# Kernel optimization log

Measured on AMD Instinct MI355X. Metric: run time of the kernel, lower is better.

The kernel has to match this reference:

```python
import jax, jax.numpy as jnp
import numpy as np

EMBED_DIM = 512
NUM_HEADS = 8
TGT_LEN = 2048
SRC_LEN = 2048
BSZ = 4
W_SCALE = 0.02  # keep pre-softmax logits in a sane range


def setup_inputs() -> dict:
    key = jax.random.key(0)
    ks = jax.random.split(key, 13)
    E = EMBED_DIM
    inp = {
        "query": jax.random.normal(ks[0], (TGT_LEN, BSZ, E), jnp.float32),
        "key": jax.random.normal(ks[1], (SRC_LEN, BSZ, E), jnp.float32),
        "value": jax.random.normal(ks[2], (SRC_LEN, BSZ, E), jnp.float32),
        "attn_mask": jax.random.normal(ks[3], (TGT_LEN, SRC_LEN), jnp.float32),
        # Linear params, torch layout: W is [out, in], y = x @ W.T + b
        "Wq": jax.random.normal(ks[4], (E, E), jnp.float32) * W_SCALE,
        "bq": jax.random.normal(ks[5], (E,), jnp.float32) * W_SCALE,
        "Wk": jax.random.normal(ks[6], (E, E), jnp.float32) * W_SCALE,
        "bk": jax.random.normal(ks[7], (E,), jnp.float32) * W_SCALE,
        "Wv": jax.random.normal(ks[8], (E, E), jnp.float32) * W_SCALE,
        "bv": jax.random.normal(ks[9], (E,), jnp.float32) * W_SCALE,
        "Wo": jax.random.normal(ks[10], (E, E), jnp.float32) * W_SCALE,
        "bo": jax.random.normal(ks[11], (E,), jnp.float32) * W_SCALE,
    }
    return inp


def reference(query, key, value, attn_mask, Wq, bq, Wk, bk, Wv, bv, Wo, bo):
    # QAT quant/dequant stubs are identity in float math; dropout p=0 (eval) is identity.
    T, B, E = query.shape
    S = key.shape[0]
    H = NUM_HEADS
    hd = E // H
    scale = hd ** (-0.5)

    q = query @ Wq.T + bq            # [T, B, E]
    k = key @ Wk.T + bk              # [S, B, E]
    v = value @ Wv.T + bv            # [S, B, E]

    q = q.reshape(T, B, H, hd) * scale
    k = k.reshape(S, B, H, hd)
    v = v.reshape(S, B, H, hd)

    # scores: [B, H, T, S]
    scores = jnp.einsum("tbhd,sbhd->bhts", q, k)
    scores = scores + attn_mask[None, None, :, :]  # mask_add.add (float mask)
    attn = jax.nn.softmax(scores, axis=-1)         # SegmentLUTSoftmax == softmax in float

    out = jnp.einsum("bhts,sbhd->tbhd", attn, v).reshape(T, B, E)
    out = out @ Wo.T + bo                          # out_proj

    # need_weights=True, average_attn_weights=True: mean over heads -> [B, T, S]
    attn_weights = jnp.sum(attn, axis=1) * (1.0 / H)
    return out, attn_weights
```

## Files before the change

kernel.cpp:

```cpp
#include <hip/hip_runtime.h>
#include <hip/hip_bf16.h>

#define T_LEN 2048
#define S_LEN 2048
#define BSZ   4
#define EMB   512
#define NHEAD 8
#define HDIM  64

using bf16x8 = __attribute__((ext_vector_type(8))) short;
using f32x4  = __attribute__((ext_vector_type(4))) float;

static __device__ __forceinline__ unsigned short f2bf(float x) {
    __hip_bfloat16 h = __float2bfloat16(x);
    return *reinterpret_cast<unsigned short*>(&h);
}
static __device__ __forceinline__ float bf2f(unsigned short u) {
    __hip_bfloat16 h;
    *reinterpret_cast<unsigned short*>(&h) = u;
    return __bfloat162float(h);
}
static __device__ __forceinline__ unsigned int pk2(float a, float b) {
    return (unsigned)f2bf(a) | ((unsigned)f2bf(b) << 16);
}

__global__ __launch_bounds__(256) void convert_w4(
    const float* __restrict__ W0, const float* __restrict__ W1,
    const float* __restrict__ W2, const float* __restrict__ W3,
    unsigned short* __restrict__ Hi, unsigned short* __restrict__ Lo, int n4)
{
    const int z = blockIdx.y;
    const float* X = (z == 0) ? W0 : (z == 1) ? W1 : (z == 2) ? W2 : W3;
    unsigned short* H = Hi + (size_t)z * (size_t)EMB * EMB;
    unsigned short* L = Lo + (size_t)z * (size_t)EMB * EMB;
    const int stride = gridDim.x * 256;
    for (int i = blockIdx.x * 256 + threadIdx.x; i < n4; i += stride) {
        float4 v = ((const float4*)X)[i];
        unsigned short h0 = f2bf(v.x), h1 = f2bf(v.y), h2 = f2bf(v.z), h3 = f2bf(v.w);
        uint2 ph, pg;
        ph.x = (unsigned)h0 | ((unsigned)h1 << 16);
        ph.y = (unsigned)h2 | ((unsigned)h3 << 16);
        pg.x = pk2(v.x - bf2f(h0), v.y - bf2f(h1));
        pg.y = pk2(v.z - bf2f(h2), v.w - bf2f(h3));
        ((uint2*)H)[i] = ph;
        ((uint2*)L)[i] = pg;
    }
}

template <int MODE, bool XF32, bool SPLIT>
__global__ __launch_bounds__(256) void proj_mfma(
    const float* __restrict__ Xf,
    const unsigned short* __restrict__ Xhi, const unsigned short* __restrict__ Xlo,
    const unsigned short* __restrict__ Whi, const unsigned short* __restrict__ Wlo,
    const float* __restrict__ bias,
    float* __restrict__ Yf, unsigned short* __restrict__ Yhi, float scale)
{
    const int n0 = blockIdx.x * 64;
    const int m0 = blockIdx.y * 64;

    __shared__ unsigned short whs[64 * 64];
    __shared__ unsigned short wls[SPLIT ? 64 * 64 : 1];
    __shared__ unsigned short xhs[XF32 ? 64 * 64 : 1];
    __shared__ unsigned short xls[(XF32 && SPLIT) ? 64 * 64 : 1];

    const int tid = threadIdx.x;
    const int w   = tid >> 6;
    const int l   = tid & 63;
    const int l4  = l >> 4, l15 = l & 15;
    const int sw  = (l & 7) << 4;
    char* whsb = (char*)whs;
    char* wlsb = (char*)wls;
    char* xhsb = (char*)xhs;
    char* xlsb = (char*)xls;

    const int srow = tid >> 2;
    const int schk = tid & 3;
    const size_t wbase = (size_t)(n0 + srow) * 512 + schk * 16;
    const int stw = (srow * 128 + schk * 32) ^ ((srow & 7) << 4);

    f32x4 acc[4];
    #pragma unroll
    for (int nb = 0; nb < 4; ++nb) { f32x4 z = {0.f, 0.f, 0.f, 0.f}; acc[nb] = z; }

    uint4 wh0 = *(const uint4*)(Whi + wbase);
    uint4 wh1 = *(const uint4*)(Whi + wbase + 8);
    uint4 wl0, wl1;
    if constexpr (SPLIT) {
        wl0 = *(const uint4*)(Wlo + wbase);
        wl1 = *(const uint4*)(Wlo + wbase + 8);
    }

    const size_t xfbase = (size_t)(m0 + srow) * 512 + schk * 16;
    const size_t xbase  = (size_t)(m0 + w * 16 + l15) * 512 + l4 * 8;
    float4 xp0, xp1, xp2, xp3;
    bf16x8 ah0, ah1, al0, al1;
    if constexpr (XF32) {
        xp0 = *(const float4*)(Xf + xfbase);
        xp1 = *(const float4*)(Xf + xfbase + 4);
        xp2 = *(const float4*)(Xf + xfbase + 8);
        xp3 = *(const float4*)(Xf + xfbase + 12);
    } else {
        ah0 = *(const bf16x8*)(Xhi + xbase);
        ah1 = *(const bf16x8*)(Xhi + xbase + 32);
        if constexpr (SPLIT) {
            al0 = *(const bf16x8*)(Xlo + xbase);
            al1 = *(const bf16x8*)(Xlo + xbase + 32);
        }
    }

    for (int c = 0; c < 8; ++c) {
        __syncthreads();
        *(uint4*)(whsb + stw)        = wh0;
        *(uint4*)(whsb + (stw ^ 16)) = wh1;
        if constexpr (SPLIT) {
            *(uint4*)(wlsb + stw)        = wl0;
            *(uint4*)(wlsb + (stw ^ 16)) = wl1;
        }
        if constexpr (XF32) {
            uint4 H0, H1;
            H0.x = pk2(xp0.x, xp0.y); H0.y = pk2(xp0.z, xp0.w);
            H0.z = pk2(xp1.x, xp1.y); H0.w = pk2(xp1.z, xp1.w);
            H1.x = pk2(xp2.x, xp2.y); H1.y = pk2(xp2.z, xp2.w);
            H1.z = pk2(xp3.x, xp3.y); H1.w = pk2(xp3.z, xp3.w);
            *(uint4*)(xhsb + stw)        = H0;
            *(uint4*)(xhsb + (stw ^ 16)) = H1;
            if constexpr (SPLIT) {
                uint4 L0, L1;
                L0.x = pk2(xp0.x - bf2f(f2bf(xp0.x)), xp0.y - bf2f(f2bf(xp0.y)));
                L0.y = pk2(xp0.z - bf2f(f2bf(xp0.z)), xp0.w - bf2f(f2bf(xp0.w)));
                L0.z = pk2(xp1.x - bf2f(f2bf(xp1.x)), xp1.y - bf2f(f2bf(xp1.y)));
                L0.w = pk2(xp1.z - bf2f(f2bf(xp1.z)), xp1.w - bf2f(f2bf(xp1.w)));
                L1.x = pk2(xp2.x - bf2f(f2bf(xp2.x)), xp2.y - bf2f(f2bf(xp2.y)));
                L1.y = pk2(xp2.z - bf2f(f2bf(xp2.z)), xp2.w - bf2f(f2bf(xp2.w)));
                L1.z = pk2(xp3.x - bf2f(f2bf(xp3.x)), xp3.y - bf2f(f2bf(xp3.y)));
                L1.w = pk2(xp3.z - bf2f(f2bf(xp3.z)), xp3.w - bf2f(f2bf(xp3.w)));
                *(uint4*)(xlsb + stw)        = L0;
                *(uint4*)(xlsb + (stw ^ 16)) = L1;
            }
        }
        __syncthreads();

        bf16x8 cah[2], cal[2];
        if constexpr (XF32) {
            #pragma unroll
            for (int kc = 0; kc < 2; ++kc) {
                const int aoff = (((w * 16 + l15) * 128) + kc * 64 + l4 * 16) ^ sw;
                cah[kc] = *(const bf16x8*)(xhsb + aoff);
                if constexpr (SPLIT) cal[kc] = *(const bf16x8*)(xlsb + aoff);
            }
        } else {
            cah[0] = ah0; cah[1] = ah1;
            if constexpr (SPLIT) { cal[0] = al0; cal[1] = al1; }
        }

        if (c < 7) {
            const size_t wb2 = wbase + (size_t)(c + 1) * 64;
            wh0 = *(const uint4*)(Whi + wb2);
            wh1 = *(const uint4*)(Whi + wb2 + 8);
            if constexpr (SPLIT) {
                wl0 = *(const uint4*)(Wlo + wb2);
                wl1 = *(const uint4*)(Wlo + wb2 + 8);
            }
            if constexpr (XF32) {
                const size_t xb2 = xfbase + (size_t)(c + 1) * 64;
                xp0 = *(const float4*)(Xf + xb2);
                xp1 = *(const float4*)(Xf + xb2 + 4);
                xp2 = *(const float4*)(Xf + xb2 + 8);
                xp3 = *(const float4*)(Xf + xb2 + 12);
            } else {
                const size_t xb2 = xbase + (size_t)(c + 1) * 64;
                ah0 = *(const bf16x8*)(Xhi + xb2);
                ah1 = *(const bf16x8*)(Xhi + xb2 + 32);
                if constexpr (SPLIT) {
                    al0 = *(const bf16x8*)(Xlo + xb2);
                    al1 = *(const bf16x8*)(Xlo + xb2 + 32);
                }
            }
        }

        #pragma unroll
        for (int kc = 0; kc < 2; ++kc) {
            #pragma unroll
            for (int nb = 0; nb < 4; ++nb) {
                const int off = (((nb * 16 + l15) * 128) + kc * 64 + l4 * 16) ^ sw;
                bf16x8 bh = *(const bf16x8*)(whsb + off);
                acc[nb] = __builtin_amdgcn_mfma_f32_16x16x32_bf16(cah[kc], bh, acc[nb], 0, 0, 0);
                if constexpr (SPLIT) {
                    bf16x8 bl = *(const bf16x8*)(wlsb + off);
                    acc[nb] = __builtin_amdgcn_mfma_f32_16x16x32_bf16(cah[kc], bl, acc[nb], 0, 0, 0);
                    acc[nb] = __builtin_amdgcn_mfma_f32_16x16x32_bf16(cal[kc], bh, acc[nb], 0, 0, 0);
                }
            }
        }
    }

    #pragma unroll
    for (int nb = 0; nb < 4; ++nb)
        #pragma unroll
        for (int r = 0; r < 4; ++r) {
            const int m = m0 + w * 16 + l4 * 4 + r;
            const int n = n0 + nb * 16 + l15;
            const float y = (acc[nb][r] + bias[n]) * scale;
            const size_t idx = (size_t)m * 512 + n;
            if constexpr (MODE == 0) Yf[idx] = y;
            else                     Yhi[idx] = f2bf(y);
        }
}

__global__ __launch_bounds__(256) void transpose_v(const unsigned short* __restrict__ V,
                                                   unsigned short* __restrict__ Vt)
{
    const int s0 = blockIdx.x * 64;
    const int h  = blockIdx.y, b = blockIdx.z;
    __shared__ unsigned short tile[64][72];
    const int tid = threadIdx.x;
    {
        const int r = tid >> 2, c = (tid & 3) * 16;
        const unsigned short* src = V + ((size_t)(s0 + r) * BSZ + b) * EMB + h * HDIM + c;
        uint4 u0 = *(const uint4*)(src);
        uint4 u1 = *(const uint4*)(src + 8);
        *(uint4*)&tile[r][c]     = u0;
        *(uint4*)&tile[r][c + 8] = u1;
    }
    __syncthreads();
    {
        const int d = tid >> 2, sg = tid & 3;
        unsigned int w_[8];
        #pragma unroll
        for (int j = 0; j < 8; ++j) {
            unsigned int lo = tile[sg * 16 + 2 * j][d];
            unsigned int hi = tile[sg * 16 + 2 * j + 1][d];
            w_[j] = lo | (hi << 16);
        }
        uint4 o0 = {w_[0], w_[1], w_[2], w_[3]};
        uint4 o1 = {w_[4], w_[5], w_[6], w_[7]};
        unsigned short* dst = Vt + ((size_t)(b * NHEAD + h) * HDIM + d) * S_LEN + s0 + sg * 16;
        *(uint4*)dst       = o0;
        *(uint4*)(dst + 8) = o1;
    }
}

__global__ __launch_bounds__(256) void flash_fwd_mfma(
    const unsigned short* __restrict__ Qbf, const unsigned short* __restrict__ Kbf,
    const unsigned short* __restrict__ Vt,  const float* __restrict__ mask,
    unsigned short* __restrict__ Ohi, unsigned short* __restrict__ Olo,
    float* __restrict__ Lout)
{
    const int tt0 = blockIdx.x * 128;
    const int h   = blockIdx.y, b = blockIdx.z;

    __shared__ unsigned short ks[2][64 * 64];
    __shared__ unsigned short vs[2][64 * 64];
    __shared__ unsigned short pl[4][2][16 * 64];

    const int tid = threadIdx.x;
    const int w   = tid >> 6;
    const int l   = tid & 63;
    const int l4  = l >> 4, l15 = l & 15;
    const int sw  = (l & 7) << 4;

    char* pb_[2] = {(char*)pl[w][0], (char*)pl[w][1]};

    bf16x8 qf[2][2];
    #pragma unroll
    for (int a = 0; a < 2; ++a) {
        const int t = tt0 + w * 32 + a * 16 + l15;
        const unsigned short* qp = Qbf + ((size_t)t * BSZ + b) * EMB + h * HDIM + l4 * 8;
        qf[a][0] = *(const bf16x8*)(qp);
        qf[a][1] = *(const bf16x8*)(qp + 32);
    }

    f32x4 oacc[2][4];
    #pragma unroll
    for (int a = 0; a < 2; ++a)
        #pragma unroll
        for (int nb = 0; nb < 4; ++nb) { f32x4 z = {0.f, 0.f, 0.f, 0.f}; oacc[a][nb] = z; }
    float lsum[2] = {0.f, 0.f};

    const int srow = tid >> 2;
    const int schk = tid & 3;
    const unsigned short* kcol = Kbf + (size_t)b * EMB + h * HDIM + schk * 16;
    const unsigned short* vrow = Vt + ((size_t)(b * NHEAD + h) * HDIM + srow) * S_LEN + schk * 16;
    const int stw = (srow * 128 + schk * 32) ^ ((srow & 7) << 4);

    const float* mrowp[2];
    #pragma unroll
    for (int a = 0; a < 2; ++a)
        mrowp[a] = mask + (size_t)(tt0 + w * 32 + a * 16 + l15) * S_LEN + l4 * 4;

    {
        const unsigned short* kp0 = kcol + (size_t)srow * BSZ * EMB;
        uint4 a0 = *(const uint4*)(kp0);
        uint4 a1 = *(const uint4*)(kp0 + 8);
        uint4 b0 = *(const uint4*)(vrow);
        uint4 b1 = *(const uint4*)(vrow + 8);
        char* k0 = (char*)ks[0];
        char* v0 = (char*)vs[0];
        *(uint4*)(k0 + stw)        = a0;
        *(uint4*)(k0 + (stw ^ 16)) = a1;
        *(uint4*)(v0 + stw)        = b0;
        *(uint4*)(v0 + (stw ^ 16)) = b1;
    }
    __syncthreads();

    uint4 ka0, ka1, va0, va1;
    const int NT = S_LEN / 64;

    for (int it = 0; it < NT; ++it) {
        const int s0  = it * 64;
        const int cur = it & 1;
        char* ksb = (char*)ks[cur];
        char* vsb = (char*)vs[cur];
        const bool haveNext = (it + 1 < NT);

        if (haveNext) {
            const unsigned short* kp2 = kcol + (size_t)(s0 + 64 + srow) * BSZ * EMB;
            ka0 = *(const uint4*)(kp2);
            ka1 = *(const uint4*)(kp2 + 8);
            va0 = *(const uint4*)(vrow + s0 + 64);
            va1 = *(const uint4*)(vrow + s0 + 64 + 8);
        }

        f32x4 sacc[2][4];
        #pragma unroll
        for (int a = 0; a < 2; ++a)
            #pragma unroll
            for (int nb = 0; nb < 4; ++nb) { f32x4 z = {0.f, 0.f, 0.f, 0.f}; sacc[a][nb] = z; }
        #pragma unroll
        for (int kc = 0; kc < 2; ++kc) {
            #pragma unroll
            for (int nb = 0; nb < 4; ++nb) {
                const int off = (((nb * 16 + l15) * 128) + kc * 64 + l4 * 16) ^ sw;
                bf16x8 kf = *(const bf16x8*)(ksb + off);
                sacc[0][nb] = __builtin_amdgcn_mfma_f32_16x16x32_bf16(kf, qf[0][kc], sacc[0][nb], 0, 0, 0);
                sacc[1][nb] = __builtin_amdgcn_mfma_f32_16x16x32_bf16(kf, qf[1][kc], sacc[1][nb], 0, 0, 0);
            }
        }

        #pragma unroll
        for (int a = 0; a < 2; ++a) {
            char* pw = pb_[a];
            #pragma unroll
            for (int nb = 0; nb < 4; ++nb) {
                float4 mk = *(const float4*)(mrowp[a] + s0 + nb * 16);
                const float p0 = __expf(sacc[a][nb][0] + mk.x);
                const float p1 = __expf(sacc[a][nb][1] + mk.y);
                const float p2 = __expf(sacc[a][nb][2] + mk.z);
                const float p3 = __expf(sacc[a][nb][3] + mk.w);
                lsum[a] += (p0 + p1) + (p2 + p3);
                uint2 pk;
                pk.x = pk2(p0, p1);
                pk.y = pk2(p2, p3);
                *(uint2*)(pw + ((l15 * 128 + nb * 32 + l4 * 8) ^ sw)) = pk;
            }
        }

        bf16x8 pa[2][2];
        #pragma unroll
        for (int a = 0; a < 2; ++a) {
            pa[a][0] = *(const bf16x8*)(pb_[a] + ((l15 * 128 + l4 * 16) ^ sw));
            pa[a][1] = *(const bf16x8*)(pb_[a] + ((l15 * 128 + 64 + l4 * 16) ^ sw));
        }
        #pragma unroll
        for (int nb = 0; nb < 4; ++nb) {
            const int off0 = (((nb * 16 + l15) * 128) + l4 * 16) ^ sw;
            bf16x8 vf0 = *(const bf16x8*)(vsb + off0);
            bf16x8 vf1 = *(const bf16x8*)(vsb + (off0 ^ 64));
            oacc[0][nb] = __builtin_amdgcn_mfma_f32_16x16x32_bf16(pa[0][0], vf0, oacc[0][nb], 0, 0, 0);
            oacc[0][nb] = __builtin_amdgcn_mfma_f32_16x16x32_bf16(pa[0][1], vf1, oacc[0][nb], 0, 0, 0);
            oacc[1][nb] = __builtin_amdgcn_mfma_f32_16x16x32_bf16(pa[1][0], vf0, oacc[1][nb], 0, 0, 0);
            oacc[1][nb] = __builtin_amdgcn_mfma_f32_16x16x32_bf16(pa[1][1], vf1, oacc[1][nb], 0, 0, 0);
        }

        if (haveNext) {
            char* kn = (char*)ks[cur ^ 1];
            char* vn = (char*)vs[cur ^ 1];
            *(uint4*)(kn + stw)        = ka0;
            *(uint4*)(kn + (stw ^ 16)) = ka1;
            *(uint4*)(vn + stw)        = va0;
            *(uint4*)(vn + (stw ^ 16)) = va1;
        }
        __syncthreads();
    }

    #pragma unroll
    for (int a = 0; a < 2; ++a) {
        float lfull = lsum[a];
        lfull += __shfl_xor(lfull, 16);
        lfull += __shfl_xor(lfull, 32);
        float linv[4];
        #pragma unroll
        for (int r = 0; r < 4; ++r)
            linv[r] = 1.0f / __shfl(lfull, l4 * 4 + r);

        #pragma unroll
        for (int nb = 0; nb < 4; ++nb)
            #pragma unroll
            for (int r = 0; r < 4; ++r) {
                const int t = tt0 + w * 32 + a * 16 + l4 * 4 + r;
                const size_t idx = ((size_t)t * BSZ + b) * EMB + h * HDIM + nb * 16 + l15;
                const float y = oacc[a][nb][r] * linv[r];
                const unsigned short hi = f2bf(y);
                Ohi[idx] = hi;
                Olo[idx] = f2bf(y - bf2f(hi));
            }
        if (l < 16)
            Lout[((size_t)b * NHEAD + h) * T_LEN + tt0 + w * 32 + a * 16 + l] = lfull;
    }
}

__global__ __launch_bounds__(256) void attn_weights_mfma(
    const unsigned short* __restrict__ Qhi, const unsigned short* __restrict__ Khi,
    const float* __restrict__ mask, const float* __restrict__ Lin,
    float* __restrict__ Wout)
{
    const int tt0 = blockIdx.x * 128;
    const int ss0 = blockIdx.y * 64;
    const int b   = blockIdx.z;

    __shared__ unsigned short khs[2][64 * 64];
    __shared__ float lls[NHEAD][128];

    const int tid = threadIdx.x;
    const int w   = tid >> 6;
    const int l   = tid & 63;
    const int l4  = l >> 4, l15 = l & 15;
    const int sw  = (l & 7) << 4;

    for (int i = tid; i < NHEAD * 128; i += 256) {
        const int hh = i >> 7, t2 = i & 127;
        lls[hh][t2] = 1.0f / Lin[(size_t)(b * NHEAD + hh) * T_LEN + tt0 + t2];
    }

    float4 msk[2][4];
    #pragma unroll
    for (int a = 0; a < 2; ++a) {
        const float* mrowp = mask + (size_t)(tt0 + w * 32 + a * 16 + l15) * S_LEN + ss0 + l4 * 4;
        #pragma unroll
        for (int nb = 0; nb < 4; ++nb) msk[a][nb] = *(const float4*)(mrowp + nb * 16);
    }

    float4 wacc[2][4] = {};

    const int srow = tid >> 2;
    const int schk = tid & 3;
    const size_t kbase = ((size_t)(ss0 + srow) * BSZ + b) * EMB + schk * 16;
    const int stw = (srow * 128 + schk * 32) ^ ((srow & 7) << 4);
    size_t qbase[2];
    #pragma unroll
    for (int a = 0; a < 2; ++a)
        qbase[a] = ((size_t)(tt0 + w * 32 + a * 16 + l15) * BSZ + b) * EMB + l4 * 8;

    {
        uint4 a0 = *(const uint4*)(Khi + kbase);
        uint4 a1 = *(const uint4*)(Khi + kbase + 8);
        char* k0 = (char*)khs[0];
        *(uint4*)(k0 + stw)        = a0;
        *(uint4*)(k0 + (stw ^ 16)) = a1;
    }
    __syncthreads();

    uint4 kh0, kh1;

    for (int h = 0; h < NHEAD; ++h) {
        const int cur = h & 1;
        char* khsb = (char*)khs[cur];
        const bool haveNext = (h + 1 < NHEAD);

        if (haveNext) {
            kh0 = *(const uint4*)(Khi + kbase + (h + 1) * HDIM);
            kh1 = *(const uint4*)(Khi + kbase + (h + 1) * HDIM + 8);
        }

        bf16x8 qh[2][2];
        #pragma unroll
        for (int a = 0; a < 2; ++a) {
            qh[a][0] = *(const bf16x8*)(Qhi + qbase[a] + h * HDIM);
            qh[a][1] = *(const bf16x8*)(Qhi + qbase[a] + h * HDIM + 32);
        }

        f32x4 sacc[2][4];
        #pragma unroll
        for (int a = 0; a < 2; ++a)
            #pragma unroll
            for (int nb = 0; nb < 4; ++nb) { f32x4 z = {0.f, 0.f, 0.f, 0.f}; sacc[a][nb] = z; }
        #pragma unroll
        for (int kc = 0; kc < 2; ++kc) {
            #pragma unroll
            for (int nb = 0; nb < 4; ++nb) {
                const int off = (((nb * 16 + l15) * 128) + kc * 64 + l4 * 16) ^ sw;
                bf16x8 kf = *(const bf16x8*)(khsb + off);
                sacc[0][nb] = __builtin_amdgcn_mfma_f32_16x16x32_bf16(kf, qh[0][kc], sacc[0][nb], 0, 0, 0);
                sacc[1][nb] = __builtin_amdgcn_mfma_f32_16x16x32_bf16(kf, qh[1][kc], sacc[1][nb], 0, 0, 0);
            }
        }

        #pragma unroll
        for (int a = 0; a < 2; ++a) {
            const float lh = lls[h][w * 32 + a * 16 + l15];
            #pragma unroll
            for (int nb = 0; nb < 4; ++nb) {
                wacc[a][nb].x += __expf(sacc[a][nb][0] + msk[a][nb].x) * lh;
                wacc[a][nb].y += __expf(sacc[a][nb][1] + msk[a][nb].y) * lh;
                wacc[a][nb].z += __expf(sacc[a][nb][2] + msk[a][nb].z) * lh;
                wacc[a][nb].w += __expf(sacc[a][nb][3] + msk[a][nb].w) * lh;
            }
        }

        if (haveNext) {
            char* kn = (char*)khs[cur ^ 1];
            *(uint4*)(kn + stw)        = kh0;
            *(uint4*)(kn + (stw ^ 16)) = kh1;
        }
        __syncthreads();
    }

    #pragma unroll
    for (int a = 0; a < 2; ++a) {
        float* orow = Wout + ((size_t)b * T_LEN + tt0 + w * 32 + a * 16 + l15) * S_LEN + ss0 + l4 * 4;
        #pragma unroll
        for (int nb = 0; nb < 4; ++nb) {
            float4 o = {wacc[a][nb].x * (1.0f / NHEAD), wacc[a][nb].y * (1.0f / NHEAD),
                        wacc[a][nb].z * (1.0f / NHEAD), wacc[a][nb].w * (1.0f / NHEAD)};
            *(float4*)(orow + nb * 16) = o;
        }
    }
}

extern "C" void kernel_launch(void* const* d_in, const int* in_sizes, int n_in,
                              void* d_out, int out_size, void* d_ws, size_t ws_size,
                              hipStream_t stream)
{
    const float* query = (const float*)d_in[0];
    const float* key   = (const float*)d_in[1];
    const float* value = (const float*)d_in[2];
    const float* mask  = (const float*)d_in[3];
    const float* Wq    = (const float*)d_in[4];
    const float* bq    = (const float*)d_in[5];
    const float* Wk    = (const float*)d_in[6];
    const float* bk    = (const float*)d_in[7];
    const float* Wv    = (const float*)d_in[8];
    const float* bv    = (const float*)d_in[9];
    const float* Wo    = (const float*)d_in[10];
    const float* bo    = (const float*)d_in[11];

    float* out = (float*)d_out;

    const size_t NQKV = (size_t)T_LEN * BSZ * EMB;
    const size_t NW   = (size_t)EMB * EMB;

    unsigned short* qhi = (unsigned short*)d_ws;
    unsigned short* khi = qhi + NQKV;
    unsigned short* vhi = khi + NQKV;
    unsigned short* whb = vhi + NQKV;
    unsigned short* wlb = whb + 4 * NW;
    float* lb = (float*)(wlb + 4 * NW);

    unsigned short* wqh = whb + 0 * NW;
    unsigned short* wkh = whb + 1 * NW;
    unsigned short* wvh = whb + 2 * NW;
    unsigned short* woh = whb + 3 * NW, *wol = wlb + 3 * NW;

    unsigned short* vt  = (unsigned short*)(out + NQKV);
    unsigned short* cxh = (unsigned short*)(out + NQKV + 3000000);
    unsigned short* cxl = (unsigned short*)(out + NQKV + 6000000);

    const dim3 gproj(8, 128);

    convert_w4<<<dim3(64, 4), 256, 0, stream>>>(Wq, Wk, Wv, Wo, whb, wlb, (int)(NW / 4));

    proj_mfma<2, true, false><<<gproj, 256, 0, stream>>>(query, nullptr, nullptr, wqh, nullptr,
                                                         bq, nullptr, qhi, 0.125f);
    proj_mfma<2, true, false><<<gproj, 256, 0, stream>>>(key, nullptr, nullptr, wkh, nullptr,
                                                         bk, nullptr, khi, 1.0f);
    proj_mfma<2, true, false><<<gproj, 256, 0, stream>>>(value, nullptr, nullptr, wvh, nullptr,
                                                         bv, nullptr, vhi, 1.0f);

    transpose_v<<<dim3(S_LEN / 64, NHEAD, BSZ), 256, 0, stream>>>(vhi, vt);

    flash_fwd_mfma<<<dim3(T_LEN / 128, NHEAD, BSZ), 256, 0, stream>>>(
        qhi, khi, vt, mask, cxh, cxl, lb);

    proj_mfma<0, false, true><<<gproj, 256, 0, stream>>>(nullptr, cxh, cxl, woh, wol, bo,
                                                         out, nullptr, 1.0f);

    attn_weights_mfma<<<dim3(T_LEN / 128, S_LEN / 64, BSZ), 256, 0, stream>>>(
        qhi, khi, mask, lb, out + NQKV);
}
```

Before: 274.3 us.

## Fold log2e into Q scale, use exp2, single-buffer K/V LDS in flash kernel

Folds log2(e) into the query projection scale so the softmax uses the native exp2 instruction, with the mask scaled by log2e via an fma or a pre-multiply. The flash kernel drops its double-buffered K/V shared memory for a single buffer, still prefetching into registers, with two barriers per tile. The 1/NHEAD factor moves into the per-row inverse sum so the final scaling multiply disappears. Single buffering halves K/V LDS and may raise occupancy, but it adds a barrier per iteration and less overlap.

Result: faster. 249.7 us (-9.0%).

```diff
diff --git a/kernel.cpp b/kernel.cpp
--- a/kernel.cpp
+++ b/kernel.cpp
@@ -7,6 +7,7 @@
 #define EMB   512
 #define NHEAD 8
 #define HDIM  64
+#define L2E   1.44269504088896f
 
 using bf16x8 = __attribute__((ext_vector_type(8))) short;
 using f32x4  = __attribute__((ext_vector_type(4))) float;
@@ -249,8 +250,8 @@
     const int tt0 = blockIdx.x * 128;
     const int h   = blockIdx.y, b = blockIdx.z;
 
-    __shared__ unsigned short ks[2][64 * 64];
-    __shared__ unsigned short vs[2][64 * 64];
+    __shared__ unsigned short ks[64 * 64];
+    __shared__ unsigned short vs[64 * 64];
     __shared__ unsigned short pl[4][2][16 * 64];
 
     const int tid = threadIdx.x;
@@ -259,6 +260,8 @@
     const int l4  = l >> 4, l15 = l & 15;
     const int sw  = (l & 7) << 4;
 
+    char* ksb = (char*)ks;
+    char* vsb = (char*)vs;
     char* pb_[2] = {(char*)pl[w][0], (char*)pl[w][1]};
 
     bf16x8 qf[2][2];
@@ -288,32 +291,21 @@
     for (int a = 0; a < 2; ++a)
         mrowp[a] = mask + (size_t)(tt0 + w * 32 + a * 16 + l15) * S_LEN + l4 * 4;
 
-    {
-        const unsigned short* kp0 = kcol + (size_t)srow * BSZ * EMB;
-        uint4 a0 = *(const uint4*)(kp0);
-        uint4 a1 = *(const uint4*)(kp0 + 8);
-        uint4 b0 = *(const uint4*)(vrow);
-        uint4 b1 = *(const uint4*)(vrow + 8);
-        char* k0 = (char*)ks[0];
-        char* v0 = (char*)vs[0];
-        *(uint4*)(k0 + stw)        = a0;
-        *(uint4*)(k0 + (stw ^ 16)) = a1;
-        *(uint4*)(v0 + stw)        = b0;
-        *(uint4*)(v0 + (stw ^ 16)) = b1;
-    }
-    __syncthreads();
-
-    uint4 ka0, ka1, va0, va1;
-    const int NT = S_LEN / 64;
-
-    for (int it = 0; it < NT; ++it) {
-        const int s0  = it * 64;
-        const int cur = it & 1;
-        char* ksb = (char*)ks[cur];
-        char* vsb = (char*)vs[cur];
-        const bool haveNext = (it + 1 < NT);
-
-        if (haveNext) {
+    const unsigned short* kp0 = kcol + (size_t)srow * BSZ * EMB;
+    uint4 ka0 = *(const uint4*)(kp0);
+    uint4 ka1 = *(const uint4*)(kp0 + 8);
+    uint4 va0 = *(const uint4*)(vrow);
+    uint4 va1 = *(const uint4*)(vrow + 8);
+
+    for (int s0 = 0; s0 < S_LEN; s0 += 64) {
+        __syncthreads();
+        *(uint4*)(ksb + stw)        = ka0;
+        *(uint4*)(ksb + (stw ^ 16)) = ka1;
+        *(uint4*)(vsb + stw)        = va0;
+        *(uint4*)(vsb + (stw ^ 16)) = va1;
+        __syncthreads();
+
+        if (s0 + 64 < S_LEN) {
             const unsigned short* kp2 = kcol + (size_t)(s0 + 64 + srow) * BSZ * EMB;
             ka0 = *(const uint4*)(kp2);
             ka1 = *(const uint4*)(kp2 + 8);
@@ -343,10 +335,10 @@
             #pragma unroll
             for (int nb = 0; nb < 4; ++nb) {
                 float4 mk = *(const float4*)(mrowp[a] + s0 + nb * 16);
-                const float p0 = __expf(sacc[a][nb][0] + mk.x);
-                const float p1 = __expf(sacc[a][nb][1] + mk.y);
-                const float p2 = __expf(sacc[a][nb][2] + mk.z);
-                const float p3 = __expf(sacc[a][nb][3] + mk.w);
+                const float p0 = __builtin_amdgcn_exp2f(fmaf(mk.x, L2E, sacc[a][nb][0]));
+                const float p1 = __builtin_amdgcn_exp2f(fmaf(mk.y, L2E, sacc[a][nb][1]));
+                const float p2 = __builtin_amdgcn_exp2f(fmaf(mk.z, L2E, sacc[a][nb][2]));
+                const float p3 = __builtin_amdgcn_exp2f(fmaf(mk.w, L2E, sacc[a][nb][3]));
                 lsum[a] += (p0 + p1) + (p2 + p3);
                 uint2 pk;
                 pk.x = pk2(p0, p1);
@@ -371,16 +363,6 @@
             oacc[1][nb] = __builtin_amdgcn_mfma_f32_16x16x32_bf16(pa[1][0], vf0, oacc[1][nb], 0, 0, 0);
             oacc[1][nb] = __builtin_amdgcn_mfma_f32_16x16x32_bf16(pa[1][1], vf1, oacc[1][nb], 0, 0, 0);
         }
-
-        if (haveNext) {
-            char* kn = (char*)ks[cur ^ 1];
-            char* vn = (char*)vs[cur ^ 1];
-            *(uint4*)(kn + stw)        = ka0;
-            *(uint4*)(kn + (stw ^ 16)) = ka1;
-            *(uint4*)(vn + stw)        = va0;
-            *(uint4*)(vn + (stw ^ 16)) = va1;
-        }
-        __syncthreads();
     }
 
     #pragma unroll
@@ -429,7 +411,7 @@
 
     for (int i = tid; i < NHEAD * 128; i += 256) {
         const int hh = i >> 7, t2 = i & 127;
-        lls[hh][t2] = 1.0f / Lin[(size_t)(b * NHEAD + hh) * T_LEN + tt0 + t2];
+        lls[hh][t2] = (1.0f / NHEAD) / Lin[(size_t)(b * NHEAD + hh) * T_LEN + tt0 + t2];
     }
 
     float4 msk[2][4];
@@ -439,6 +421,13 @@
         #pragma unroll
         for (int nb = 0; nb < 4; ++nb) msk[a][nb] = *(const float4*)(mrowp + nb * 16);
     }
+    #pragma unroll
+    for (int a = 0; a < 2; ++a)
+        #pragma unroll
+        for (int nb = 0; nb < 4; ++nb) {
+            msk[a][nb].x *= L2E; msk[a][nb].y *= L2E;
+            msk[a][nb].z *= L2E; msk[a][nb].w *= L2E;
+        }
 
     float4 wacc[2][4] = {};
 
@@ -500,10 +489,10 @@
             const float lh = lls[h][w * 32 + a * 16 + l15];
             #pragma unroll
             for (int nb = 0; nb < 4; ++nb) {
-                wacc[a][nb].x += __expf(sacc[a][nb][0] + msk[a][nb].x) * lh;
-                wacc[a][nb].y += __expf(sacc[a][nb][1] + msk[a][nb].y) * lh;
-                wacc[a][nb].z += __expf(sacc[a][nb][2] + msk[a][nb].z) * lh;
-                wacc[a][nb].w += __expf(sacc[a][nb][3] + msk[a][nb].w) * lh;
+                wacc[a][nb].x += __builtin_amdgcn_exp2f(sacc[a][nb][0] + msk[a][nb].x) * lh;
+                wacc[a][nb].y += __builtin_amdgcn_exp2f(sacc[a][nb][1] + msk[a][nb].y) * lh;
+                wacc[a][nb].z += __builtin_amdgcn_exp2f(sacc[a][nb][2] + msk[a][nb].z) * lh;
+                wacc[a][nb].w += __builtin_amdgcn_exp2f(sacc[a][nb][3] + msk[a][nb].w) * lh;
             }
         }
 
@@ -519,11 +508,8 @@
     for (int a = 0; a < 2; ++a) {
         float* orow = Wout + ((size_t)b * T_LEN + tt0 + w * 32 + a * 16 + l15) * S_LEN + ss0 + l4 * 4;
         #pragma unroll
-        for (int nb = 0; nb < 4; ++nb) {
-            float4 o = {wacc[a][nb].x * (1.0f / NHEAD), wacc[a][nb].y * (1.0f / NHEAD),
-                        wacc[a][nb].z * (1.0f / NHEAD), wacc[a][nb].w * (1.0f / NHEAD)};
-            *(float4*)(orow + nb * 16) = o;
-        }
+        for (int nb = 0; nb < 4; ++nb)
+            *(float4*)(orow + nb * 16) = wacc[a][nb];
     }
 }
 
@@ -570,7 +556,7 @@
     convert_w4<<<dim3(64, 4), 256, 0, stream>>>(Wq, Wk, Wv, Wo, whb, wlb, (int)(NW / 4));
 
     proj_mfma<2, true, false><<<gproj, 256, 0, stream>>>(query, nullptr, nullptr, wqh, nullptr,
-                                                         bq, nullptr, qhi, 0.125f);
+                                                         bq, nullptr, qhi, 0.125f * L2E);
     proj_mfma<2, true, false><<<gproj, 256, 0, stream>>>(key, nullptr, nullptr, wkh, nullptr,
                                                          bk, nullptr, khi, 1.0f);
     proj_mfma<2, true, false><<<gproj, 256, 0, stream>>>(value, nullptr, nullptr, wvh, nullptr,
```
